# Kernel tuning notes

Measured on AMD Instinct MI355X. Metric: run time of the kernel, lower is better.

Reference implementation:

```python
import jax, jax.numpy as jnp
import numpy as np

H = 64
N_TYPES = 20
EDGE_DIM = 4
N_GRAPHS = 128
N_LAYERS = 3
N_NODES = 50000
N_EDGES = 800000
NQ = 4

# ---- quantum-circuit constants (4 qubits, statevector of 16) ----
def _cnot_mat(c, t, n=NQ):
    m = np.zeros((2**n, 2**n), np.complex64)
    for i in range(2**n):
        bits = [(i >> (n - 1 - k)) & 1 for k in range(n)]
        jb = list(bits)
        if bits[c]:
            jb[t] ^= 1
        j = sum(b << (n - 1 - k) for k, b in enumerate(jb))
        m[j, i] = 1.0
    return m

CNOTS = jnp.array(np.stack([_cnot_mat(q, (q + 1) % NQ) for q in range(NQ)]))
ZSIGN = jnp.array(np.array([[1.0 - 2.0 * ((i >> (NQ - 1 - q)) & 1) for i in range(2**NQ)] for q in range(NQ)], np.float32))
I2 = np.eye(2, dtype=np.complex64)

def _rx(t):
    c = jnp.cos(t / 2).astype(jnp.complex64)
    s = jnp.sin(t / 2).astype(jnp.complex64)
    return jnp.stack([jnp.stack([c, -1j * s]), jnp.stack([-1j * s, c])])

def _ry(t):
    c = jnp.cos(t / 2)
    s = jnp.sin(t / 2)
    return jnp.stack([jnp.stack([c, -s]), jnp.stack([s, c])]).astype(jnp.complex64)

def _full1q(g, q):
    ops = [jnp.asarray(I2)] * NQ
    ops[q] = g
    m = ops[0]
    for o in ops[1:]:
        m = jnp.kron(m, o)
    return m

def _circuit(x, w):
    # x: [4] input angles, w: [n_layers=2, 4] RY weights
    psi = jnp.zeros(2**NQ, jnp.complex64).at[0].set(1.0)
    for q in range(NQ):
        psi = _full1q(_rx(x[q]), q) @ psi
    for l in range(w.shape[0]):
        for q in range(NQ):
            psi = _full1q(_ry(w[l, q]), q) @ psi
        for q in range(NQ):
            psi = CNOTS[q] @ psi
    probs = jnp.abs(psi) ** 2
    return ZSIGN @ probs  # PauliZ expval per qubit, [4]

def _forward(node_types, edge_index, batch, pos, edge_attr, emb, ew1, eb1, ew2, eb2,
             cw1, cb1, cw2, cb2, nw1, nb1, nw2, nb2, prew, preb, qw, pw1, pb1, pw2, pb2):
    silu = jax.nn.silu
    n = pos.shape[0]
    src, dst = edge_index[0], edge_index[1]
    deg = jnp.maximum(jax.ops.segment_sum(jnp.ones((src.shape[0],), pos.dtype), dst, num_segments=n), 1.0)[:, None]
    h = emb[node_types]  # [N, H]
    for l in range(N_LAYERS):
        rel = pos[dst] - pos[src]                      # [E, 3]
        d2 = jnp.sum(rel * rel, axis=-1, keepdims=True)  # [E, 1]
        m_in = jnp.concatenate([h[dst], h[src], d2, edge_attr], axis=-1)  # [E, 2H+1+edge_dim]
        m = silu(m_in @ ew1[l] + eb1[l])
        m = silu(m @ ew2[l] + eb2[l])                  # [E, H] messages
        c = silu(m @ cw1[l] + cb1[l]) @ cw2[l] + cb2[l]  # [E, 1] coord scalar
        pos = pos + jax.ops.segment_sum(rel * c, dst, num_segments=n) / deg
        agg = jax.ops.segment_sum(m, dst, num_segments=n)  # [N, H]
        h = h + silu(jnp.concatenate([h, agg], axis=-1) @ nw1[l] + nb1[l]) @ nw2[l] + nb2[l]
    # global mean pool over graphs
    cnt = jnp.maximum(jax.ops.segment_sum(jnp.ones((n,), h.dtype), batch, num_segments=N_GRAPHS), 1.0)[:, None]
    g = jax.ops.segment_sum(h, batch, num_segments=N_GRAPHS) / cnt  # [G, H]
    q_in = g @ prew + preb                              # [G, 4]
    q_out = jax.vmap(lambda x: _circuit(x, qw))(q_in)   # [G, 4]
    return silu(q_out @ pw1 + pb1) @ pw2 + pb2          # [G, 1]

def setup_inputs() -> dict:
    key = jax.random.key(0)
    ks = jax.random.split(key, 20)
    def lin(k, i, o, layers=None):
        shape = (i, o) if layers is None else (layers, i, o)
        return (jax.random.normal(k, shape, jnp.float32) / np.sqrt(i))
    return {
        "node_types": jax.random.randint(ks[0], (N_NODES,), 0, N_TYPES),
        "pos": jax.random.normal(ks[1], (N_NODES, 3), jnp.float32),
        "edge_index": jax.random.randint(ks[2], (2, N_EDGES), 0, N_NODES),
        "edge_attr": jax.random.normal(ks[3], (N_EDGES, EDGE_DIM), jnp.float32),
        "batch": jnp.sort(jax.random.randint(ks[4], (N_NODES,), 0, N_GRAPHS)),
        "emb": jax.random.normal(ks[5], (N_TYPES, H), jnp.float32),
        "ew1": lin(ks[6], 2 * H + 1 + EDGE_DIM, H, N_LAYERS), "eb1": jnp.zeros((N_LAYERS, H), jnp.float32),
        "ew2": lin(ks[7], H, H, N_LAYERS), "eb2": jnp.zeros((N_LAYERS, H), jnp.float32),
        "cw1": lin(ks[8], H, H, N_LAYERS), "cb1": jnp.zeros((N_LAYERS, H), jnp.float32),
        "cw2": lin(ks[9], H, 1, N_LAYERS) * 0.1, "cb2": jnp.zeros((N_LAYERS, 1), jnp.float32),
        "nw1": lin(ks[10], 2 * H, H, N_LAYERS), "nb1": jnp.zeros((N_LAYERS, H), jnp.float32),
        "nw2": lin(ks[11], H, H, N_LAYERS), "nb2": jnp.zeros((N_LAYERS, H), jnp.float32),
        "prew": lin(ks[12], H, NQ), "preb": jnp.zeros((NQ,), jnp.float32),
        "qw": jax.random.uniform(ks[13], (2, NQ), jnp.float32, 0.0, 2.0 * np.pi),
        "pw1": lin(ks[14], NQ, H), "pb1": jnp.zeros((H,), jnp.float32),
        "pw2": lin(ks[15], H, 1), "pb2": jnp.zeros((1,), jnp.float32),
    }

def reference(node_types, pos, edge_index, edge_attr, batch, emb, ew1, eb1, ew2, eb2,
              cw1, cb1, cw2, cb2, nw1, nb1, nw2, nb2, prew, preb, qw, pw1, pb1, pw2, pb2):
    return _forward(node_types, edge_index, batch, pos, edge_attr, emb, ew1, eb1, ew2, eb2,
                    cw1, cb1, cw2, cb2, nw1, nb1, nw2, nb2, prew, preb, qw, pw1, pb1, pw2, pb2)
```

## Files before the change

kernel.cpp:

```cpp
#include <hip/hip_runtime.h>

#define NN 50000
#define NE 800000
#define NG 128
#define NL 3
#define NGRP (NE / 16)

typedef __attribute__((ext_vector_type(8))) short short8;
typedef __attribute__((ext_vector_type(4))) float f32x4;
typedef __attribute__((ext_vector_type(4))) int i32x4;

union FragU { i32x4 i; short8 s; };

__device__ __forceinline__ float silu_f(float x) { return x / (1.f + __expf(-x)); }
__device__ __forceinline__ float rdl(float v, int l) {
  return __int_as_float(__builtin_amdgcn_readlane(__float_as_int(v), l));
}
__device__ __forceinline__ float wave_sum(float v) {
#pragma unroll
  for (int m = 1; m < 64; m <<= 1) v += __shfl_xor(v, m, 64);
  return v;
}

__device__ __forceinline__ unsigned f2u(float x) { return __float_as_uint(x); }
__device__ __forceinline__ float hi_part(float x) {
  return __uint_as_float(f2u(x) & 0xffff0000u);
}
__device__ __forceinline__ unsigned pk_hi(float e0, float e1) {
  return __builtin_amdgcn_perm(f2u(e1), f2u(e0), 0x07060302u);
}

__device__ __forceinline__ f32x4 mfma16(i32x4 a, i32x4 b, f32x4 c) {
  FragU ua, ub; ua.i = a; ub.i = b;
  return __builtin_amdgcn_mfma_f32_16x16x32_bf16(ua.s, ub.s, c, 0, 0, 0);
}

__device__ __forceinline__ void split8(const float* x, i32x4& fh, i32x4& fl) {
#pragma unroll
  for (int i = 0; i < 4; ++i) {
    const float a = x[2 * i], b = x[2 * i + 1];
    fh[i] = (int)pk_hi(a, b);
    fl[i] = (int)pk_hi(a - hi_part(a), b - hi_part(b));
  }
}

__device__ __forceinline__ void wfrag(const float* __restrict__ W, int nrows, int k0,
                                      int n, int lane, i32x4& fh, i32x4& fl) {
  const int kb = k0 + ((lane >> 4) << 3);
  float x[8];
#pragma unroll
  for (int j = 0; j < 8; ++j) {
    const int k = kb + j;
    x[j] = (k < nrows) ? W[k * 64 + n] : 0.f;
  }
  split8(x, fh, fl);
}

__global__ __launch_bounds__(256) void k_init_h(const int* __restrict__ nt,
                                                const float* __restrict__ emb,
                                                float* __restrict__ h,
                                                unsigned short* __restrict__ hpk) {
  int idx = blockIdx.x * 256 + threadIdx.x;
  if (idx < NN * 64) {
    const int node = idx >> 6, c = idx & 63;
    const float v = emb[nt[node] * 64 + c];
    h[idx] = v;
    const unsigned hb = f2u(v) & 0xffff0000u;
    const float lo = v - __uint_as_float(hb);
    hpk[node * 128 + c] = (unsigned short)(hb >> 16);
    hpk[node * 128 + 64 + c] = (unsigned short)(f2u(lo) >> 16);
  }
}

__global__ __launch_bounds__(256) void k_prep(const float* __restrict__ pos_in,
                                              float* __restrict__ pos,
                                              float* __restrict__ deg,
                                              float* __restrict__ g,
                                              float* __restrict__ gcnt,
                                              float* __restrict__ agg,
                                              float* __restrict__ posd) {
  int idx = blockIdx.x * 256 + threadIdx.x;
  if (idx < NN * 64) agg[idx] = 0.f;
  if (idx < NN * 3) { pos[idx] = pos_in[idx]; posd[idx] = 0.f; }
  if (idx < NN) deg[idx] = 0.f;
  if (idx < NG * 64) g[idx] = 0.f;
  if (idx < NG) gcnt[idx] = 0.f;
}

__global__ __launch_bounds__(256) void k_hist(const int* __restrict__ ei,
                                              float* __restrict__ deg) {
  int e = blockIdx.x * 256 + threadIdx.x;
  if (e < NE) atomicAdd(&deg[ei[NE + e]], 1.f);
}

__global__ __launch_bounds__(256) void k_cnt(const int* __restrict__ batch,
                                             float* __restrict__ deg,
                                             float* __restrict__ gcnt) {
  int i = blockIdx.x * 256 + threadIdx.x;
  if (i < NN) {
    deg[i] = fmaxf(deg[i], 1.f);
    atomicAdd(&gcnt[batch[i]], 1.f);
  }
}

__global__ __launch_bounds__(256) void k_pos(float* __restrict__ pos,
                                             float* __restrict__ posd,
                                             const float* __restrict__ deg) {
  int idx = blockIdx.x * 256 + threadIdx.x;
  if (idx < NN * 3) {
    pos[idx] += posd[idx] / deg[idx / 3];
    posd[idx] = 0.f;
  }
}

__global__ __launch_bounds__(256) void k_pool(const float* __restrict__ h,
                                              const int* __restrict__ batch,
                                              float* __restrict__ g) {
  const int lane = threadIdx.x & 63;
  const int wid = (blockIdx.x * 256 + threadIdx.x) >> 6;
  const int nw = (gridDim.x * 256) >> 6;
  for (int n0 = wid * 16; n0 < NN; n0 += nw * 16) {
    float acc = 0.f;
    int curb = batch[n0];
#pragma unroll
    for (int i = 0; i < 16; ++i) {
      const int b = batch[n0 + i];
      const float v = h[(size_t)(n0 + i) * 64 + lane];
      if (b != curb) {
        atomicAdd(&g[curb * 64 + lane], acc);
        acc = 0.f;
        curb = b;
      }
      acc += v;
    }
    atomicAdd(&g[curb * 64 + lane], acc);
  }
}

__global__ __launch_bounds__(768, 3) void k_edge(
    const unsigned short* __restrict__ hpk, const float* __restrict__ pos,
    const int* __restrict__ ei, const float* __restrict__ eattr,
    const float* __restrict__ W1, const float* __restrict__ B1,
    const float* __restrict__ W2, const float* __restrict__ B2,
    const float* __restrict__ C1, const float* __restrict__ CB1,
    const float* __restrict__ C2, const float* __restrict__ CB2,
    float* __restrict__ agg, float* __restrict__ posd) {
  __shared__ i32x4 smem[7680];

  const int tid = threadIdx.x;
  const int lane = tid & 63;
  const int w = tid >> 6;
  const int m = lane & 15;
  const int quad = lane >> 4;

  for (int j = w; j < 36; j += 12) {
    int s, t, nrows, hb, lb;
    const float* W;
    if (j < 20)      { s = j >> 2; t = j & 3; W = W1; nrows = 133; hb = 0; lb = 1280; }
    else if (j < 28) { const int q = j - 20; s = q >> 2; t = q & 3; W = W2; nrows = 64; hb = 2560; lb = 3072; }
    else             { const int q = j - 28; s = q >> 2; t = q & 3; W = C1; nrows = 64; hb = 3584; lb = 4096; }
    i32x4 fh, fl;
    wfrag(W, nrows, 32 * s, t * 16 + m, lane, fh, fl);
    smem[hb + (s * 4 + t) * 64 + lane] = fh;
    smem[lb + (s * 4 + t) * 64 + lane] = fl;
  }
  __syncthreads();

  float eb1t[4], eb2t[4], cb1t[4], cw2t[4];
#pragma unroll
  for (int t = 0; t < 4; ++t) {
    eb1t[t] = B1[t * 16 + m];
    eb2t[t] = B2[t * 16 + m];
    cb1t[t] = CB1[t * 16 + m];
    cw2t[t] = C2[t * 16 + m];
  }
  const float cb2v = CB2[0];

  char* pl = (char*)(smem + 4608) + w * 4096;
  const char* hB = (const char*)hpk;

  const int gw0 = blockIdx.x * 12 + w;
  const int nwv = gridDim.x * 12;

  int es = 0, ed = 0;
  if (gw0 < NGRP) {
    es = ei[gw0 * 16 + m];
    ed = ei[NE + gw0 * 16 + m];
  }

#define STORE_PAIR(base, row, toff, v)                                          \
  {                                                                             \
    const float vp_ = __shfl_xor((v), 1, 64);                                   \
    if (!(m & 1)) {                                                             \
      const int off_ = (row) * 128 + ((((toff) + m * 2)) ^ (((row) & 7) << 4)); \
      *(unsigned*)((base) + off_) = pk_hi((v), vp_);                            \
      *(unsigned*)((base) + 2048 + off_) =                                      \
          pk_hi((v)-hi_part(v), vp_ - hi_part(vp_));                            \
    }                                                                           \
  }

  for (int g = gw0; g < NGRP; g += nwv) {
    const int e0 = g * 16;
    const int ces = es, ced = ed;
    const int g2 = g + nwv;
    if (g2 < NGRP) {
      es = ei[g2 * 16 + m];
      ed = ei[NE + g2 * 16 + m];
    }

    i32x4 fh[4], fl[4];
#pragma unroll
    for (int s = 0; s < 4; ++s) {
      const unsigned node = (unsigned)(s < 2 ? ced : ces);
      const unsigned off = node * 256u + (unsigned)((s & 1) * 64 + quad * 16);
      fh[s] = *(const i32x4*)(hB + off);
      fl[s] = *(const i32x4*)(hB + off + 128);
    }

    float rx = 0.f, ry = 0.f, rz = 0.f, d2v = 0.f;
    float ea0 = 0.f, ea1 = 0.f, ea2 = 0.f, ea3 = 0.f;
    if (lane < 16) {
      rx = pos[ced * 3 + 0] - pos[ces * 3 + 0];
      ry = pos[ced * 3 + 1] - pos[ces * 3 + 1];
      rz = pos[ced * 3 + 2] - pos[ces * 3 + 2];
      d2v = rx * rx + ry * ry + rz * rz;
      const float4 ea = *(const float4*)(eattr + 4 * (e0 + lane));
      ea0 = ea.x; ea1 = ea.y; ea2 = ea.z; ea3 = ea.w;
    }

    i32x4 th, tl;
    {
      float x0 = __shfl(d2v, m), x1 = __shfl(ea0, m), x2 = __shfl(ea1, m),
            x3 = __shfl(ea2, m), x4 = __shfl(ea3, m);
      if (quad) { x0 = x1 = x2 = x3 = x4 = 0.f; }
      float xt[8] = {x0, x1, x2, x3, x4, 0.f, 0.f, 0.f};
      split8(xt, th, tl);
    }

#pragma unroll
    for (int t = 0; t < 4; ++t) {
      f32x4 P = {eb1t[t], eb1t[t], eb1t[t], eb1t[t]}, Q = {0.f, 0.f, 0.f, 0.f};
#pragma unroll
      for (int s = 0; s < 4; ++s) {
        const i32x4 wh = smem[(s * 4 + t) * 64 + lane];
        const i32x4 wl = smem[1280 + (s * 4 + t) * 64 + lane];
        P = mfma16(fh[s], wh, P);
        Q = mfma16(fh[s], wl, Q);
        Q = mfma16(fl[s], wh, Q);
      }
      {
        const i32x4 wh = smem[(16 + t) * 64 + lane];
        const i32x4 wl = smem[1280 + (16 + t) * 64 + lane];
        P = mfma16(th, wh, P);
        Q = mfma16(th, wl, Q);
        Q = mfma16(tl, wh, Q);
      }
#pragma unroll
      for (int r = 0; r < 4; ++r) {
        const int row = quad * 4 + r;
        const float v = silu_f(P[r] + Q[r]);
        STORE_PAIR(pl, row, t * 32, v);
      }
    }

    int rd[4];
#pragma unroll
    for (int r = 0; r < 4; ++r) rd[r] = __shfl(ced, quad * 4 + r, 64);

    i32x4 ah[2], al[2];
#pragma unroll
    for (int s = 0; s < 2; ++s) {
      const int off = m * 128 + ((s * 64 + quad * 16) ^ ((m & 7) << 4));
      ah[s] = *(const i32x4*)(pl + off);
      al[s] = *(const i32x4*)(pl + 2048 + off);
    }
#pragma unroll
    for (int t = 0; t < 4; ++t) {
      f32x4 P = {eb2t[t], eb2t[t], eb2t[t], eb2t[t]}, Q = {0.f, 0.f, 0.f, 0.f};
#pragma unroll
      for (int s = 0; s < 2; ++s) {
        const i32x4 wh = smem[2560 + (s * 4 + t) * 64 + lane];
        const i32x4 wl = smem[3072 + (s * 4 + t) * 64 + lane];
        P = mfma16(ah[s], wh, P);
        Q = mfma16(ah[s], wl, Q);
        Q = mfma16(al[s], wh, Q);
      }
#pragma unroll
      for (int r = 0; r < 4; ++r) {
        const int row = quad * 4 + r;
        const float mv = silu_f(P[r] + Q[r]);
        STORE_PAIR(pl, row, t * 32, mv);
        atomicAdd(&agg[(size_t)rd[r] * 64 + t * 16 + m], mv);
      }
    }

    i32x4 mh[2], ml[2];
#pragma unroll
    for (int s = 0; s < 2; ++s) {
      const int off = m * 128 + ((s * 64 + quad * 16) ^ ((m & 7) << 4));
      mh[s] = *(const i32x4*)(pl + off);
      ml[s] = *(const i32x4*)(pl + 2048 + off);
    }
    float tr[4] = {0.f, 0.f, 0.f, 0.f};
#pragma unroll
    for (int t = 0; t < 4; ++t) {
      f32x4 P = {cb1t[t], cb1t[t], cb1t[t], cb1t[t]}, Q = {0.f, 0.f, 0.f, 0.f};
#pragma unroll
      for (int s = 0; s < 2; ++s) {
        const i32x4 wh = smem[3584 + (s * 4 + t) * 64 + lane];
        const i32x4 wl = smem[4096 + (s * 4 + t) * 64 + lane];
        P = mfma16(mh[s], wh, P);
        Q = mfma16(mh[s], wl, Q);
        Q = mfma16(ml[s], wh, Q);
      }
#pragma unroll
      for (int r = 0; r < 4; ++r) tr[r] += silu_f(P[r] + Q[r]) * cw2t[t];
    }
#pragma unroll
    for (int mask = 1; mask < 16; mask <<= 1)
#pragma unroll
      for (int r = 0; r < 4; ++r) tr[r] += __shfl_xor(tr[r], mask, 64);

    {
      const int rr = m >> 2, cc = m & 3;
      const int e = quad * 4 + rr;
      const float tv = ((rr & 2) ? ((rr & 1) ? tr[3] : tr[2])
                                 : ((rr & 1) ? tr[1] : tr[0])) + cb2v;
      const int d_ = __shfl(ced, e, 64);
      const float ax = __shfl(rx, e, 64), ay = __shfl(ry, e, 64),
                  az = __shfl(rz, e, 64);
      if (cc < 3) {
        const float rel = cc == 0 ? ax : (cc == 1 ? ay : az);
        atomicAdd(&posd[d_ * 3 + cc], rel * tv);
      }
    }
  }
#undef STORE_PAIR
}

__global__ __launch_bounds__(256) void k_node(
    float* __restrict__ h, unsigned short* __restrict__ hpk,
    float* __restrict__ agg,
    const float* __restrict__ W1, const float* __restrict__ B1,
    const float* __restrict__ W2, const float* __restrict__ B2) {
  __shared__ float sW1[128 * 64];
  __shared__ float sW2[64 * 64];
  for (int i = threadIdx.x; i < 128 * 64; i += 256) sW1[i] = W1[i];
  for (int i = threadIdx.x; i < 64 * 64; i += 256) sW2[i] = W2[i];
  __syncthreads();
  const int lane = threadIdx.x & 63;
  const float nb1 = B1[lane], nb2 = B2[lane];
  const int wid = (blockIdx.x * 256 + threadIdx.x) >> 6;
  const int nw = (gridDim.x * 256) >> 6;
  for (int n0 = wid * 8; n0 < NN; n0 += nw * 8) {
    float hj[8], aj[8], a1[8];
#pragma unroll
    for (int i = 0; i < 8; ++i) {
      hj[i] = h[(size_t)(n0 + i) * 64 + lane];
      aj[i] = agg[(size_t)(n0 + i) * 64 + lane];
      a1[i] = nb1;
    }
#pragma unroll
    for (int i = 0; i < 8; ++i) agg[(size_t)(n0 + i) * 64 + lane] = 0.f;
#pragma unroll
    for (int k = 0; k < 64; ++k) {
      const float wv = sW1[k * 64 + lane];
#pragma unroll
      for (int i = 0; i < 8; ++i) a1[i] += rdl(hj[i], k) * wv;
    }
#pragma unroll
    for (int k = 0; k < 64; ++k) {
      const float wv = sW1[(64 + k) * 64 + lane];
#pragma unroll
      for (int i = 0; i < 8; ++i) a1[i] += rdl(aj[i], k) * wv;
    }
    float u[8], a2[8];
#pragma unroll
    for (int i = 0; i < 8; ++i) { u[i] = silu_f(a1[i]); a2[i] = nb2; }
#pragma unroll
    for (int k = 0; k < 64; ++k) {
      const float wv = sW2[k * 64 + lane];
#pragma unroll
      for (int i = 0; i < 8; ++i) a2[i] += rdl(u[i], k) * wv;
    }
#pragma unroll
    for (int i = 0; i < 8; ++i) {
      const float hn = hj[i] + a2[i];
      h[(size_t)(n0 + i) * 64 + lane] = hn;
      const unsigned hb = f2u(hn) & 0xffff0000u;
      const float lo = hn - __uint_as_float(hb);
      hpk[(size_t)(n0 + i) * 128 + lane] = (unsigned short)(hb >> 16);
      hpk[(size_t)(n0 + i) * 128 + 64 + lane] = (unsigned short)(f2u(lo) >> 16);
    }
  }
}

__global__ __launch_bounds__(256) void k_final(
    const float* __restrict__ g, const float* __restrict__ gcnt,
    const float* __restrict__ prew, const float* __restrict__ preb,
    const float* __restrict__ qw, const float* __restrict__ pw1,
    const float* __restrict__ pb1, const float* __restrict__ pw2,
    const float* __restrict__ pb2, float* __restrict__ out) {
  const int lane = threadIdx.x & 63;
  const int gid = (blockIdx.x * 256 + threadIdx.x) >> 6;
  if (gid >= NG) return;
  const float cnt = fmaxf(gcnt[gid], 1.f);
  const float gv = g[gid * 64 + lane] / cnt;
  float qin[4];
#pragma unroll
  for (int q = 0; q < 4; ++q)
    qin[q] = wave_sum(gv * prew[lane * 4 + q]) + preb[q];
  float sr[16], si[16];
#pragma unroll
  for (int i = 0; i < 16; ++i) { sr[i] = 0.f; si[i] = 0.f; }
  sr[0] = 1.f;
#pragma unroll
  for (int q = 0; q < 4; ++q) {
    const int mask = 8 >> q;
    float s, c;
    __sincosf(qin[q] * 0.5f, &s, &c);
#pragma unroll
    for (int i = 0; i < 16; ++i)
      if (!(i & mask)) {
        const int j = i | mask;
        const float ar = sr[i], ai = si[i], br = sr[j], bi = si[j];
        sr[i] = c * ar + s * bi; si[i] = c * ai - s * br;
        sr[j] = c * br + s * ai; si[j] = c * bi - s * ar;
      }
  }
#pragma unroll
  for (int l = 0; l < 2; ++l) {
#pragma unroll
    for (int q = 0; q < 4; ++q) {
      const int mask = 8 >> q;
      float s, c;
      __sincosf(qw[l * 4 + q] * 0.5f, &s, &c);
#pragma unroll
      for (int i = 0; i < 16; ++i)
        if (!(i & mask)) {
          const int j = i | mask;
          const float ar = sr[i], ai = si[i], br = sr[j], bi = si[j];
          sr[i] = c * ar - s * br; si[i] = c * ai - s * bi;
          sr[j] = s * ar + c * br; si[j] = s * ai + c * bi;
        }
    }
#pragma unroll
    for (int q = 0; q < 4; ++q) {
      const int mc = 8 >> q;
      const int mt = 8 >> ((q + 1) & 3);
#pragma unroll
      for (int i = 0; i < 16; ++i)
        if ((i & mc) && !(i & mt)) {
          const int j = i | mt;
          float t = sr[i]; sr[i] = sr[j]; sr[j] = t;
          t = si[i]; si[i] = si[j]; si[j] = t;
        }
    }
  }
  float qo[4] = {0.f, 0.f, 0.f, 0.f};
#pragma unroll
  for (int i = 0; i < 16; ++i) {
    const float p = sr[i] * sr[i] + si[i] * si[i];
#pragma unroll
    for (int q = 0; q < 4; ++q) qo[q] += ((i >> (3 - q)) & 1) ? -p : p;
  }
  float t = pb1[lane];
#pragma unroll
  for (int q = 0; q < 4; ++q) t += qo[q] * pw1[q * 64 + lane];
  const float r = wave_sum(silu_f(t) * pw2[lane]);
  if (lane == 0) out[gid] = r + pb2[0];
}

extern "C" void kernel_launch(void* const* d_in, const int* in_sizes, int n_in,
                              void* d_out, int out_size, void* d_ws, size_t ws_size,
                              hipStream_t stream) {
  (void)in_sizes; (void)n_in; (void)out_size; (void)ws_size;
  const int*   nt    = (const int*)d_in[0];
  const float* pos0  = (const float*)d_in[1];
  const int*   ei    = (const int*)d_in[2];
  const float* eattr = (const float*)d_in[3];
  const int*   batch = (const int*)d_in[4];
  const float* emb   = (const float*)d_in[5];
  const float* ew1   = (const float*)d_in[6];
  const float* eb1   = (const float*)d_in[7];
  const float* ew2   = (const float*)d_in[8];
  const float* eb2   = (const float*)d_in[9];
  const float* cw1   = (const float*)d_in[10];
  const float* cb1   = (const float*)d_in[11];
  const float* cw2   = (const float*)d_in[12];
  const float* cb2   = (const float*)d_in[13];
  const float* nw1   = (const float*)d_in[14];
  const float* nb1   = (const float*)d_in[15];
  const float* nw2   = (const float*)d_in[16];
  const float* nb2   = (const float*)d_in[17];
  const float* prew  = (const float*)d_in[18];
  const float* preb  = (const float*)d_in[19];
  const float* qw    = (const float*)d_in[20];
  const float* pw1   = (const float*)d_in[21];
  const float* pb1   = (const float*)d_in[22];
  const float* pw2   = (const float*)d_in[23];
  const float* pb2   = (const float*)d_in[24];
  float* out = (float*)d_out;

  float* ws   = (float*)d_ws;
  float* h    = ws;
  float* pos  = h + NN * 64;
  float* posd = pos + NN * 3;
  float* agg  = posd + NN * 3;
  float* deg  = agg + NN * 64;
  float* g    = deg + NN;
  float* gcnt = g + NG * 64;
  unsigned short* hpk = (unsigned short*)(gcnt + NG);

  k_init_h<<<(NN * 64 + 255) / 256, 256, 0, stream>>>(nt, emb, h, hpk);
  k_prep<<<(NN * 64 + 255) / 256, 256, 0, stream>>>(pos0, pos, deg, g, gcnt,
                                                    agg, posd);
  k_hist<<<(NE + 255) / 256, 256, 0, stream>>>(ei, deg);
  k_cnt<<<(NN + 255) / 256, 256, 0, stream>>>(batch, deg, gcnt);
  for (int l = 0; l < NL; ++l) {
    k_edge<<<256, 768, 0, stream>>>(hpk, pos, ei, eattr,
        ew1 + l * 133 * 64, eb1 + l * 64, ew2 + l * 64 * 64, eb2 + l * 64,
        cw1 + l * 64 * 64, cb1 + l * 64, cw2 + l * 64, cb2 + l, agg, posd);
    k_pos<<<(NN * 3 + 255) / 256, 256, 0, stream>>>(pos, posd, deg);
    k_node<<<512, 256, 0, stream>>>(h, hpk, agg, nw1 + l * 128 * 64, nb1 + l * 64,
                                    nw2 + l * 64 * 64, nb2 + l * 64);
  }
  k_pool<<<800, 256, 0, stream>>>(h, batch, g);
  k_final<<<(NG * 64 + 255) / 256, 256, 0, stream>>>(g, gcnt, prew, preb, qw,
                                                     pw1, pb1, pw2, pb2, out);
}
```

Before: 1.184 ms.

## Sort edges by destination and pre-reduce message atomics per destination run

Adds a one-time counting sort of edges by destination (a histogram already exists, plus a single-block scan and an atomic scatter of src, dst and edge attributes). The edge kernel then walks contiguous chunks of sorted edges and sums messages within each 16-edge group that share a destination before issuing one atomicAdd per run. The aim is fewer and less contended global atomics on agg and better locality for destination gathers. The cost is the extra preprocessing kernels, a serial single-block scan, and a ballot/shuffle loop per group. Because the scatter uses atomics, edge order within each destination is nondeterministic, so float summation order can differ between runs.

```diff
diff --git a/kernel.cpp b/kernel.cpp
--- a/kernel.cpp
+++ b/kernel.cpp
@@ -93,6 +93,59 @@
   if (e < NE) atomicAdd(&deg[ei[NE + e]], 1.f);
 }
 
+__global__ __launch_bounds__(1024) void k_scan(const float* __restrict__ deg,
+                                               int* __restrict__ rowptr,
+                                               int* __restrict__ cursor) {
+  __shared__ int wsum[16];
+  __shared__ int s_carry;
+  __shared__ int s_total;
+  const int tid = threadIdx.x, lane = tid & 63, w = tid >> 6;
+  if (tid == 0) s_carry = 0;
+  __syncthreads();
+  const int nch = (NN + 1023) / 1024;
+  for (int c = 0; c < nch; ++c) {
+    const int i = c * 1024 + tid;
+    const int v = (i < NN) ? (int)deg[i] : 0;
+    int x = v;
+#pragma unroll
+    for (int o = 1; o < 64; o <<= 1) {
+      const int y = __shfl_up(x, o, 64);
+      if (lane >= o) x += y;
+    }
+    if (lane == 63) wsum[w] = x;
+    __syncthreads();
+    if (tid == 0) {
+      int acc = 0;
+#pragma unroll
+      for (int k = 0; k < 16; ++k) { const int t = wsum[k]; wsum[k] = acc; acc += t; }
+      s_total = acc;
+    }
+    __syncthreads();
+    const int excl = s_carry + wsum[w] + (x - v);
+    if (i < NN) { rowptr[i] = excl; cursor[i] = excl; }
+    __syncthreads();
+    if (tid == 0) s_carry += s_total;
+    __syncthreads();
+  }
+  if (tid == 0) rowptr[NN] = NE;
+}
+
+__global__ __launch_bounds__(256) void k_scatter(const int* __restrict__ ei,
+                                                 const float* __restrict__ eattr,
+                                                 int* __restrict__ cursor,
+                                                 int* __restrict__ ssrc,
+                                                 int* __restrict__ sdst,
+                                                 float4* __restrict__ seattr) {
+  const int e = blockIdx.x * 256 + threadIdx.x;
+  if (e < NE) {
+    const int s = ei[e], d = ei[NE + e];
+    const int p = atomicAdd(&cursor[d], 1);
+    ssrc[p] = s;
+    sdst[p] = d;
+    seattr[p] = *(const float4*)(eattr + 4 * (size_t)e);
+  }
+}
+
 __global__ __launch_bounds__(256) void k_cnt(const int* __restrict__ batch,
                                              float* __restrict__ deg,
                                              float* __restrict__ gcnt) {
@@ -139,7 +192,8 @@
 
 __global__ __launch_bounds__(768, 3) void k_edge(
     const unsigned short* __restrict__ hpk, const float* __restrict__ pos,
-    const int* __restrict__ ei, const float* __restrict__ eattr,
+    const int* __restrict__ ssrc, const int* __restrict__ sdst,
+    const float4* __restrict__ seattr,
     const float* __restrict__ W1, const float* __restrict__ B1,
     const float* __restrict__ W2, const float* __restrict__ B2,
     const float* __restrict__ C1, const float* __restrict__ CB1,
@@ -179,13 +233,16 @@
   char* pl = (char*)(smem + 4608) + w * 4096;
   const char* hB = (const char*)hpk;
 
-  const int gw0 = blockIdx.x * 12 + w;
+  const int gw = blockIdx.x * 12 + w;
   const int nwv = gridDim.x * 12;
+  const int ipw = (NGRP + nwv - 1) / nwv;
+  const int gbeg = min(gw * ipw, NGRP);
+  const int gend = min(gbeg + ipw, NGRP);
 
   int es = 0, ed = 0;
-  if (gw0 < NGRP) {
-    es = ei[gw0 * 16 + m];
-    ed = ei[NE + gw0 * 16 + m];
+  if (gbeg < gend) {
+    es = ssrc[gbeg * 16 + m];
+    ed = sdst[gbeg * 16 + m];
   }
 
 #define STORE_PAIR(base, row, toff, v)                                          \
@@ -199,13 +256,12 @@
     }                                                                           \
   }
 
-  for (int g = gw0; g < NGRP; g += nwv) {
+  for (int g = gbeg; g < gend; ++g) {
     const int e0 = g * 16;
     const int ces = es, ced = ed;
-    const int g2 = g + nwv;
-    if (g2 < NGRP) {
-      es = ei[g2 * 16 + m];
-      ed = ei[NE + g2 * 16 + m];
+    if (g + 1 < gend) {
+      es = ssrc[(g + 1) * 16 + m];
+      ed = sdst[(g + 1) * 16 + m];
     }
 
     i32x4 fh[4], fl[4];
@@ -224,7 +280,7 @@
       ry = pos[ced * 3 + 1] - pos[ces * 3 + 1];
       rz = pos[ced * 3 + 2] - pos[ces * 3 + 2];
       d2v = rx * rx + ry * ry + rz * rz;
-      const float4 ea = *(const float4*)(eattr + 4 * (e0 + lane));
+      const float4 ea = seattr[e0 + lane];
       ea0 = ea.x; ea1 = ea.y; ea2 = ea.z; ea3 = ea.w;
     }
 
@@ -263,10 +319,6 @@
       }
     }
 
-    int rd[4];
-#pragma unroll
-    for (int r = 0; r < 4; ++r) rd[r] = __shfl(ced, quad * 4 + r, 64);
-
     i32x4 ah[2], al[2];
 #pragma unroll
     for (int s = 0; s < 2; ++s) {
@@ -274,6 +326,7 @@
       ah[s] = *(const i32x4*)(pl + off);
       al[s] = *(const i32x4*)(pl + 2048 + off);
     }
+    float mv[4][4];
 #pragma unroll
     for (int t = 0; t < 4; ++t) {
       f32x4 P = {eb2t[t], eb2t[t], eb2t[t], eb2t[t]}, Q = {0.f, 0.f, 0.f, 0.f};
@@ -288,9 +341,31 @@
 #pragma unroll
       for (int r = 0; r < 4; ++r) {
         const int row = quad * 4 + r;
-        const float mv = silu_f(P[r] + Q[r]);
-        STORE_PAIR(pl, row, t * 32, mv);
-        atomicAdd(&agg[(size_t)rd[r] * 64 + t * 16 + m], mv);
+        mv[t][r] = silu_f(P[r] + Q[r]);
+        STORE_PAIR(pl, row, t * 32, mv[t][r]);
+      }
+    }
+
+    {
+      const bool headp = (m == 0) || (ced != __shfl(ced, lane - 1, 64));
+      unsigned rem = (unsigned)(__ballot(headp) & 0xFFFFull);
+      while (rem) {
+        const int hrow = __ffs((int)rem) - 1;
+        rem &= rem - 1;
+        const int nrow = rem ? (__ffs((int)rem) - 1) : 16;
+        const int dstn = __shfl(ced, hrow, 64);
+#pragma unroll
+        for (int t = 0; t < 4; ++t) {
+          float s = 0.f;
+#pragma unroll
+          for (int r = 0; r < 4; ++r) {
+            const int row = quad * 4 + r;
+            s += (row >= hrow && row < nrow) ? mv[t][r] : 0.f;
+          }
+          s += __shfl_xor(s, 16, 64);
+          s += __shfl_xor(s, 32, 64);
+          if (quad == 0) atomicAdd(&agg[(size_t)dstn * 64 + t * 16 + m], s);
+        }
       }
     }
 
@@ -511,14 +586,22 @@
   float* g    = deg + NN;
   float* gcnt = g + NG * 64;
   unsigned short* hpk = (unsigned short*)(gcnt + NG);
+  float4* seattr = (float4*)(hpk + NN * 128);
+  int* ssrc   = (int*)(seattr + NE);
+  int* sdst   = ssrc + NE;
+  int* rowptr = sdst + NE;
+  int* cursor = rowptr + NN + 1;
 
   k_init_h<<<(NN * 64 + 255) / 256, 256, 0, stream>>>(nt, emb, h, hpk);
   k_prep<<<(NN * 64 + 255) / 256, 256, 0, stream>>>(pos0, pos, deg, g, gcnt,
                                                     agg, posd);
   k_hist<<<(NE + 255) / 256, 256, 0, stream>>>(ei, deg);
+  k_scan<<<1, 1024, 0, stream>>>(deg, rowptr, cursor);
+  k_scatter<<<(NE + 255) / 256, 256, 0, stream>>>(ei, eattr, cursor, ssrc, sdst,
+                                                  seattr);
   k_cnt<<<(NN + 255) / 256, 256, 0, stream>>>(batch, deg, gcnt);
   for (int l = 0; l < NL; ++l) {
-    k_edge<<<256, 768, 0, stream>>>(hpk, pos, ei, eattr,
+    k_edge<<<256, 768, 0, stream>>>(hpk, pos, ssrc, sdst, seattr,
         ew1 + l * 133 * 64, eb1 + l * 64, ew2 + l * 64 * 64, eb2 + l * 64,
         cw1 + l * 64 * 64, cb1 + l * 64, cw2 + l * 64, cb2 + l, agg, posd);
     k_pos<<<(NN * 3 + 255) / 256, 256, 0, stream>>>(pos, posd, deg);
```

Result: faster. 1.120 ms (-5.4%).
